# Performance work log

Hardware: AMD Instinct MI355X
Metric: run time of the kernel (lower is better)

## Reference

```python
import jax, jax.numpy as jnp
import numpy as np

B, C, H = 32, 1, 384
K = 378  # cropped size per ProbaV cPSNR spec
NSHIFT = 7  # u, v each in [0, 7)


def _crops(target):
    # 49 shifted 378x378 crops of the HR target -> [49, B, C, K, K]
    return jnp.stack([target[:, :, u:u + K, v:v + K]
                      for u in range(NSHIFT) for v in range(NSHIFT)])


def setup_inputs() -> dict:
    key = jax.random.key(0)
    k1, k2, k3 = jax.random.split(key, 3)
    # scale to [0, 255) so the HR > 5 validity mask is nontrivial
    pred = jax.random.uniform(k1, (B, C, H, H), dtype=jnp.float32) * 255.0
    target = jax.random.uniform(k2, (B, C, H, H), dtype=jnp.float32) * 255.0
    blended_target = jax.random.uniform(k3, (B, C, H, H), dtype=jnp.float32) * 255.0
    return {"pred": pred, "target": target, "blended_target": blended_target}


def reference(pred, target, blended_target):
    # SR: center crop of the super-resolved prediction
    SR = pred[:, :, 3:3 + K, 3:3 + K]                      # [B, C, K, K]
    HR = _crops(target)                                     # [49, B, C, K, K]
    mask = (HR > 5.0).astype(SR.dtype)                      # validity mask per shift
    denom = jnp.sum(mask, axis=(1, 2, 3, 4))                # [49]
    co = 1.0 / denom
    # brightness bias b per shift (masked mean of HR - SR)
    b = co * jnp.sum((HR - SR) * mask, axis=(1, 2, 3, 4))   # [49]
    diff = HR - SR - b[:, None, None, None, None]
    # NOTE: torch code sums the squared error over ALL pixels (unmasked),
    # scaled by 1/num_valid -- replicated faithfully here.
    cmses = co * jnp.sum(diff * diff, axis=(1, 2, 3, 4))    # [49]
    idx = jnp.argmin(cmses)                                  # first min, like strict '<' loop
    cMSE = cmses[idx]
    cPSNR = -10.0 * jnp.log10(cMSE)
    HR_best = HR[idx]                                        # [B, C, K, K]
    # ListedLoss('l1', reduction='mean') -> mean absolute error
    MAE = jnp.mean(jnp.abs(SR - HR_best))
    return (cPSNR, MAE)
```

## Files before the change

### kernel.cpp

```cpp
#include <hip/hip_runtime.h>
#include <math.h>

#define HH 384
#define H2 (HH*HH)
#define NIMG 32
#define KK 378
#define NSH 49
#define NTOTD 4572288.0

#define SEGW 14
#define NSEG 27
#define NSLOT 9
#define GR 2
#define TR 18
#define NTILE 21
#define NBLK1 (NIMG*NTILE)
#define NACT (NSEG*NSLOT)
#define LDS_STRIDE 386

typedef float v2f __attribute__((ext_vector_type(2)));

#define OFF_PART   0
#define OFF_ROWOUT (OFF_PART + 100*NBLK1)
#define OFF_HEAD   (OFF_ROWOUT + 12288*52)
#define OFF_TAIL   (OFF_HEAD + 32*7*6*4)
#define OFF_COLSUM (OFF_TAIL + 32*7*6*4)
#define OFF_MISC   (OFF_COLSUM + 224*4*2)

__device__ __forceinline__ float wred(float x) {
    x += __int_as_float(__builtin_amdgcn_update_dpp(0, __float_as_int(x), 0x111, 0xf, 0xf, true));
    x += __int_as_float(__builtin_amdgcn_update_dpp(0, __float_as_int(x), 0x112, 0xf, 0xf, true));
    x += __int_as_float(__builtin_amdgcn_update_dpp(0, __float_as_int(x), 0x114, 0xf, 0xf, true));
    x += __int_as_float(__builtin_amdgcn_update_dpp(0, __float_as_int(x), 0x118, 0xf, 0xf, true));
    x += __int_as_float(__builtin_amdgcn_update_dpp(0, __float_as_int(x), 0x142, 0xa, 0xf, true));
    x += __int_as_float(__builtin_amdgcn_update_dpp(0, __float_as_int(x), 0x143, 0xc, 0xf, true));
    return x;
}

__global__ __launch_bounds__(256) void k_corr(
    const float* __restrict__ pred, const float* __restrict__ targ,
    float* __restrict__ part)
{
    __shared__ v2f lds_t[(TR + 6) * LDS_STRIDE];
    __shared__ float red[100];

    const int bid = blockIdx.x;
    const int img = bid / NTILE;
    const int tile = bid - img * NTILE;
    const int r0 = tile * TR;
    const int tid = threadIdx.x;
    const int lane = tid & 63;

    if (tid < 100) red[tid] = 0.0f;

    const float* timg = targ + (size_t)img * H2;
    for (int k = 0; k < 9; ++k) {
        int i = tid + k * 256;
        int r = i / 96, c4 = (i - r * 96) * 4;
        const float4 t4 = *reinterpret_cast<const float4*>(timg + (r0 + r) * HH + c4);
        int base = r * LDS_STRIDE + c4;
        lds_t[base + 0] = (v2f){t4.x, t4.x > 5.0f ? 1.0f : 0.0f};
        lds_t[base + 1] = (v2f){t4.y, t4.y > 5.0f ? 1.0f : 0.0f};
        lds_t[base + 2] = (v2f){t4.z, t4.z > 5.0f ? 1.0f : 0.0f};
        lds_t[base + 3] = (v2f){t4.w, t4.w > 5.0f ? 1.0f : 0.0f};
    }

    const bool valid = tid < NACT;
    int seg  = valid ? tid % NSEG : NSEG - 1;
    int slot = valid ? tid / NSEG : NSLOT - 1;
    const int c0 = seg * SEGW;
    const int slot2 = slot * GR;

    float p_[GR][SEGW];
    float sp = 0.0f, sp2 = 0.0f;
    const float* pimg = pred + (size_t)img * H2;
#pragma unroll
    for (int dr = 0; dr < GR; ++dr) {
        const float* prow = pimg + (size_t)(3 + r0 + slot2 + dr) * HH + 3 + c0;
#pragma unroll
        for (int c = 0; c < SEGW; ++c) {
            float pv = prow[c];
            p_[dr][c] = pv;
            sp += pv;
            sp2 = fmaf(pv, pv, sp2);
        }
    }

    v2f acc[NSH];
#pragma unroll
    for (int i = 0; i < NSH; ++i) acc[i] = (v2f){0.0f, 0.0f};

    __syncthreads();

#pragma unroll
    for (int g = 0; g < GR + 6; ++g) {
        v2f win[SEGW + 6];
        const int wbase = (slot2 + g) * LDS_STRIDE + c0;
#pragma unroll
        for (int c = 0; c < SEGW + 6; ++c) win[c] = lds_t[wbase + c];
#pragma unroll
        for (int dr = 0; dr < GR; ++dr) {
            const int u = g - dr;
            if (u < 0 || u > 6) continue;
#pragma unroll
            for (int c = 0; c < SEGW; ++c) {
                const float pv = p_[dr][c];
                const v2f pvv = (v2f){pv, pv};
#pragma unroll
                for (int v = 0; v < 7; ++v)
                    acc[u * 7 + v] += win[v + c] * pvv;
            }
        }
        __builtin_amdgcn_sched_barrier(0);
    }

    const float vf = valid ? 1.0f : 0.0f;
    sp *= vf; sp2 *= vf;
#pragma unroll
    for (int i = 0; i < NSH; ++i) {
        float rx = wred(acc[i].x * vf);
        float ry = wred(acc[i].y * vf);
        if (lane == 63) { atomicAdd(&red[2 * i], rx); atomicAdd(&red[2 * i + 1], ry); }
    }
    {
        float rs = wred(sp), rs2 = wred(sp2);
        if (lane == 63) { atomicAdd(&red[98], rs); atomicAdd(&red[99], rs2); }
    }
    __syncthreads();
    if (tid < 100) part[(size_t)tid * NBLK1 + bid] = red[tid];
}

__global__ __launch_bounds__(256) void k_rows(
    const float* __restrict__ targ, float* __restrict__ rowout)
{
    const int tid = threadIdx.x;
    const int w = tid >> 6, lane = tid & 63;
    const int row = blockIdx.x * 4 + w;
    const int img = row / HH, y = row - img * HH;
    const float* tr = targ + (size_t)img * H2 + (size_t)y * HH;
    float* ro = rowout + (size_t)row * 52;

    float s0 = 0, s1 = 0, s2 = 0, s3 = 0;
#pragma unroll
    for (int j = 0; j < 6; ++j) {
        int x = lane + 64 * j;
        float t = tr[x];
        float m = t > 5.0f ? 1.0f : 0.0f;
        float t2 = t * t, tm = t * m;
        s0 += t; s1 += t2; s2 += tm; s3 += m;
        if (j == 0 && lane < 6) {
            ro[4 + x * 4 + 0] = t; ro[4 + x * 4 + 1] = t2;
            ro[4 + x * 4 + 2] = tm; ro[4 + x * 4 + 3] = m;
        }
        if (j == 5 && lane >= 58) {
            int k = x - 378;
            ro[28 + k * 4 + 0] = t; ro[28 + k * 4 + 1] = t2;
            ro[28 + k * 4 + 2] = tm; ro[28 + k * 4 + 3] = m;
        }
    }
    s0 = wred(s0); s1 = wred(s1); s2 = wred(s2); s3 = wred(s3);
    if (lane == 63) { ro[0] = s0; ro[1] = s1; ro[2] = s2; ro[3] = s3; }
}

__global__ __launch_bounds__(256) void k_cols(
    const float* __restrict__ rowout, double* __restrict__ colsum,
    float* __restrict__ headw, float* __restrict__ tailw)
{
    __shared__ double sd[256][4];
    const int img = blockIdx.x / 7, v = blockIdx.x - img * 7;
    const int tid = threadIdx.x;
    double a[4] = {0, 0, 0, 0};

    for (int y = tid; y < HH; y += 256) {
        const float* rp = rowout + ((size_t)img * HH + y) * 52;
        float rw[4];
#pragma unroll
        for (int q = 0; q < 4; ++q) rw[q] = rp[q];
        for (int j = 0; j < v; ++j)
#pragma unroll
            for (int q = 0; q < 4; ++q) rw[q] -= rp[4 + j * 4 + q];
        for (int k = v; k < 6; ++k)
#pragma unroll
            for (int q = 0; q < 4; ++q) rw[q] -= rp[28 + k * 4 + q];
#pragma unroll
        for (int q = 0; q < 4; ++q) a[q] += (double)rw[q];
        if (y < 6) {
#pragma unroll
            for (int q = 0; q < 4; ++q)
                headw[(((size_t)img * 7 + v) * 6 + y) * 4 + q] = rw[q];
        }
        if (y >= KK) {
#pragma unroll
            for (int q = 0; q < 4; ++q)
                tailw[(((size_t)img * 7 + v) * 6 + (y - KK)) * 4 + q] = rw[q];
        }
    }
#pragma unroll
    for (int q = 0; q < 4; ++q) sd[tid][q] = a[q];
    __syncthreads();
    if (tid < 4) {
        double t = 0;
        for (int i = 0; i < 256; ++i) t += sd[i][tid];
        colsum[((size_t)img * 7 + v) * 4 + tid] = t;
    }
}

__global__ __launch_bounds__(256) void k_comb(
    const float* __restrict__ part, const double* __restrict__ colsum,
    const float* __restrict__ headw, const float* __restrict__ tailw,
    float* __restrict__ out, int* __restrict__ misc)
{
    __shared__ double sd[200];
    __shared__ double corrD[100];
    __shared__ double Wd[NSH][4];
    const int tid = threadIdx.x;

    if (tid < 200) {
        int i = tid >> 1, h = tid & 1;
        const float* pp = part + (size_t)i * NBLK1 + h * 336;
        double s = 0;
        for (int b = 0; b < 336; ++b) s += (double)pp[b];
        sd[tid] = s;
    }
    __syncthreads();
    if (tid < 100) corrD[tid] = sd[2 * tid] + sd[2 * tid + 1];

    if (tid < 196) {
        int s = tid >> 2, q = tid & 3;
        int u = s / 7, v = s - u * 7;
        double a = 0;
        for (int img = 0; img < NIMG; ++img) {
            a += colsum[((size_t)img * 7 + v) * 4 + q];
            const float* hw = headw + (((size_t)img * 7 + v) * 6) * 4;
            const float* tw = tailw + (((size_t)img * 7 + v) * 6) * 4;
            for (int y = 0; y < u; ++y) a -= (double)hw[y * 4 + q];
            for (int k = u; k < 6; ++k) a -= (double)tw[k * 4 + q];
        }
        Wd[s][q] = a;
    }
    __syncthreads();

    if (tid == 0) {
        const double Sp = corrD[98], Sp2 = corrD[99];
        double best = 1e300; int bi = 0;
        for (int s = 0; s < NSH; ++s) {
            double tp = corrD[2 * s], mp = corrD[2 * s + 1];
            double Wt = Wd[s][0], Wt2 = Wd[s][1], Wtm = Wd[s][2], cnt = Wd[s][3];
            double b = (Wtm - mp) / cnt;
            double s1 = Wt - Sp;
            double s2t = Wt2 - 2.0 * tp + Sp2;
            double cmse = (s2t - 2.0 * b * s1 + NTOTD * b * b) / cnt;
            if (cmse < best) { best = cmse; bi = s; }
        }
        out[0] = (float)(-10.0 * log10(best));
        out[1] = 0.0f;
        misc[0] = bi;
    }
}

__global__ __launch_bounds__(256) void k_mae(
    const float* __restrict__ pred, const float* __restrict__ targ,
    const int* __restrict__ misc, float* __restrict__ out)
{
    __shared__ float ps[4];
    const int idx = misc[0];
    const int u = idx / 7, v = idx - u * 7;
    const int tid = threadIdx.x;
    const int lane = tid & 63, w = tid >> 6;
    const int total = NIMG * KK * KK;
    float s = 0.0f;
    for (int i = blockIdx.x * 256 + tid; i < total; i += gridDim.x * 256) {
        int img = i / (KK * KK);
        int rem = i - img * (KK * KK);
        int r = rem / KK, c = rem - r * KK;
        float t = targ[(size_t)img * H2 + (size_t)(r + u) * HH + (c + v)];
        float p = pred[(size_t)img * H2 + (size_t)(r + 3) * HH + (c + 3)];
        s += fabsf(t - p);
    }
    s = wred(s);
    if (lane == 63) ps[w] = s;
    __syncthreads();
    if (tid == 0)
        atomicAdd(&out[1], (ps[0] + ps[1] + ps[2] + ps[3]) * (float)(1.0 / NTOTD));
}

extern "C" void kernel_launch(void* const* d_in, const int* in_sizes, int n_in,
                              void* d_out, int out_size, void* d_ws, size_t ws_size,
                              hipStream_t stream) {
    const float* pred = (const float*)d_in[0];
    const float* targ = (const float*)d_in[1];
    float* w = (float*)d_ws;
    float* part    = w + OFF_PART;
    float* rowout  = w + OFF_ROWOUT;
    float* headw   = w + OFF_HEAD;
    float* tailw   = w + OFF_TAIL;
    double* colsum = (double*)(w + OFF_COLSUM);
    int*   misc    = (int*)(w + OFF_MISC);
    float* out = (float*)d_out;

    k_corr<<<NBLK1, 256, 0, stream>>>(pred, targ, part);
    k_rows<<<12288 / 4, 256, 0, stream>>>(targ, rowout);
    k_cols<<<NIMG * 7, 256, 0, stream>>>(rowout, colsum, headw, tailw);
    k_comb<<<1, 256, 0, stream>>>(part, colsum, headw, tailw, out, misc);
    k_mae<<<1024, 256, 0, stream>>>(pred, targ, misc, out);
}
```

Before: 222.0 us.

## Parallelize final reductions across blocks and move shift-window sums into column kernel

The single-block combine kernel, which serially summed 672 partials per correlation term and looped over images and head/tail rows, is split up. A new 100-block reduction kernel now sums the correlation partials. The column kernel now uses 384 threads, one per row, with vectorized float4 loads and a tree reduction in LDS. It also computes the per-shift window sums directly, and a small final kernel picks the argmin. This targets the serial tail latency of the one-block kernel, at the cost of an extra kernel launch and more double-precision LDS traffic.

```diff
diff --git a/kernel.cpp b/kernel.cpp
--- a/kernel.cpp
+++ b/kernel.cpp
@@ -22,10 +22,9 @@
 
 #define OFF_PART   0
 #define OFF_ROWOUT (OFF_PART + 100*NBLK1)
-#define OFF_HEAD   (OFF_ROWOUT + 12288*52)
-#define OFF_TAIL   (OFF_HEAD + 32*7*6*4)
-#define OFF_COLSUM (OFF_TAIL + 32*7*6*4)
-#define OFF_MISC   (OFF_COLSUM + 224*4*2)
+#define OFF_WPART  (OFF_ROWOUT + 12288*52)
+#define OFF_CORRD  (OFF_WPART + 12544)
+#define OFF_MISC   (OFF_CORRD + 200)
 
 __device__ __forceinline__ float wred(float x) {
     x += __int_as_float(__builtin_amdgcn_update_dpp(0, __float_as_int(x), 0x111, 0xf, 0xf, true));
@@ -162,96 +161,103 @@
     if (lane == 63) { ro[0] = s0; ro[1] = s1; ro[2] = s2; ro[3] = s3; }
 }
 
-__global__ __launch_bounds__(256) void k_cols(
-    const float* __restrict__ rowout, double* __restrict__ colsum,
-    float* __restrict__ headw, float* __restrict__ tailw)
-{
-    __shared__ double sd[256][4];
+__global__ __launch_bounds__(384) void k_cols(
+    const float* __restrict__ rowout, double* __restrict__ wpart)
+{
+    __shared__ double sd[384][4];
+    __shared__ float hb[6][4], tb[6][4];
     const int img = blockIdx.x / 7, v = blockIdx.x - img * 7;
-    const int tid = threadIdx.x;
-    double a[4] = {0, 0, 0, 0};
-
-    for (int y = tid; y < HH; y += 256) {
-        const float* rp = rowout + ((size_t)img * HH + y) * 52;
-        float rw[4];
-#pragma unroll
-        for (int q = 0; q < 4; ++q) rw[q] = rp[q];
-        for (int j = 0; j < v; ++j)
-#pragma unroll
-            for (int q = 0; q < 4; ++q) rw[q] -= rp[4 + j * 4 + q];
-        for (int k = v; k < 6; ++k)
-#pragma unroll
-            for (int q = 0; q < 4; ++q) rw[q] -= rp[28 + k * 4 + q];
-#pragma unroll
-        for (int q = 0; q < 4; ++q) a[q] += (double)rw[q];
-        if (y < 6) {
-#pragma unroll
-            for (int q = 0; q < 4; ++q)
-                headw[(((size_t)img * 7 + v) * 6 + y) * 4 + q] = rw[q];
-        }
-        if (y >= KK) {
-#pragma unroll
-            for (int q = 0; q < 4; ++q)
-                tailw[(((size_t)img * 7 + v) * 6 + (y - KK)) * 4 + q] = rw[q];
-        }
-    }
-#pragma unroll
-    for (int q = 0; q < 4; ++q) sd[tid][q] = a[q];
-    __syncthreads();
-    if (tid < 4) {
-        double t = 0;
-        for (int i = 0; i < 256; ++i) t += sd[i][tid];
-        colsum[((size_t)img * 7 + v) * 4 + tid] = t;
-    }
-}
-
-__global__ __launch_bounds__(256) void k_comb(
-    const float* __restrict__ part, const double* __restrict__ colsum,
-    const float* __restrict__ headw, const float* __restrict__ tailw,
+    const int y = threadIdx.x;
+
+    const float* rp = rowout + ((size_t)img * HH + y) * 52;
+    float4 r4[13];
+#pragma unroll
+    for (int i = 0; i < 13; ++i) r4[i] = reinterpret_cast<const float4*>(rp)[i];
+    const float* rf = reinterpret_cast<const float*>(r4);
+
+    float rw[4];
+#pragma unroll
+    for (int q = 0; q < 4; ++q) rw[q] = rf[q];
+    for (int j = 0; j < v; ++j)
+#pragma unroll
+        for (int q = 0; q < 4; ++q) rw[q] -= rf[4 + j * 4 + q];
+    for (int k = v; k < 6; ++k)
+#pragma unroll
+        for (int q = 0; q < 4; ++q) rw[q] -= rf[28 + k * 4 + q];
+
+#pragma unroll
+    for (int q = 0; q < 4; ++q) sd[y][q] = (double)rw[q];
+    if (y < 6)
+#pragma unroll
+        for (int q = 0; q < 4; ++q) hb[y][q] = rw[q];
+    if (y >= KK)
+#pragma unroll
+        for (int q = 0; q < 4; ++q) tb[y - KK][q] = rw[q];
+    __syncthreads();
+
+    for (int s = 192; s >= 3; s >>= 1) {
+        if (y < s)
+#pragma unroll
+            for (int q = 0; q < 4; ++q) sd[y][q] += sd[y + s][q];
+        __syncthreads();
+    }
+
+    if (y < 28) {
+        int u = y >> 2, q = y & 3;
+        double a = sd[0][q] + sd[1][q] + sd[2][q];
+        for (int j = 0; j < u; ++j) a -= (double)hb[j][q];
+        for (int k = u; k < 6; ++k) a -= (double)tb[k][q];
+        wpart[((size_t)(u * 7 + v) * 4 + q) * 32 + img] = a;
+    }
+}
+
+__global__ __launch_bounds__(256) void k_red(
+    const float* __restrict__ part, double* __restrict__ corrD)
+{
+    __shared__ double sd[256];
+    const int q = blockIdx.x;
+    const int t = threadIdx.x;
+    const float* pp = part + (size_t)q * NBLK1;
+    double a = (double)pp[t] + (double)pp[t + 256];
+    if (t < NBLK1 - 512) a += (double)pp[t + 512];
+    sd[t] = a;
+    __syncthreads();
+    for (int s = 128; s > 0; s >>= 1) {
+        if (t < s) sd[t] += sd[t + s];
+        __syncthreads();
+    }
+    if (t == 0) corrD[q] = sd[0];
+}
+
+__global__ __launch_bounds__(256) void k_fin(
+    const double* __restrict__ corrD, const double* __restrict__ wpart,
     float* __restrict__ out, int* __restrict__ misc)
 {
-    __shared__ double sd[200];
-    __shared__ double corrD[100];
     __shared__ double Wd[NSH][4];
-    const int tid = threadIdx.x;
-
-    if (tid < 200) {
-        int i = tid >> 1, h = tid & 1;
-        const float* pp = part + (size_t)i * NBLK1 + h * 336;
-        double s = 0;
-        for (int b = 0; b < 336; ++b) s += (double)pp[b];
-        sd[tid] = s;
-    }
-    __syncthreads();
-    if (tid < 100) corrD[tid] = sd[2 * tid] + sd[2 * tid + 1];
-
-    if (tid < 196) {
-        int s = tid >> 2, q = tid & 3;
-        int u = s / 7, v = s - u * 7;
-        double a = 0;
-        for (int img = 0; img < NIMG; ++img) {
-            a += colsum[((size_t)img * 7 + v) * 4 + q];
-            const float* hw = headw + (((size_t)img * 7 + v) * 6) * 4;
-            const float* tw = tailw + (((size_t)img * 7 + v) * 6) * 4;
-            for (int y = 0; y < u; ++y) a -= (double)hw[y * 4 + q];
-            for (int k = u; k < 6; ++k) a -= (double)tw[k * 4 + q];
-        }
-        Wd[s][q] = a;
-    }
-    __syncthreads();
-
-    if (tid == 0) {
-        const double Sp = corrD[98], Sp2 = corrD[99];
-        double best = 1e300; int bi = 0;
-        for (int s = 0; s < NSH; ++s) {
-            double tp = corrD[2 * s], mp = corrD[2 * s + 1];
-            double Wt = Wd[s][0], Wt2 = Wd[s][1], Wtm = Wd[s][2], cnt = Wd[s][3];
-            double b = (Wtm - mp) / cnt;
-            double s1 = Wt - Sp;
-            double s2t = Wt2 - 2.0 * tp + Sp2;
-            double cmse = (s2t - 2.0 * b * s1 + NTOTD * b * b) / cnt;
-            if (cmse < best) { best = cmse; bi = s; }
-        }
+    __shared__ double cm[NSH];
+    const int t = threadIdx.x;
+
+    if (t < 196) {
+        const double* wp = wpart + (size_t)t * 32;
+        double a0 = 0, a1 = 0;
+#pragma unroll
+        for (int i = 0; i < 32; i += 2) { a0 += wp[i]; a1 += wp[i + 1]; }
+        Wd[t >> 2][t & 3] = a0 + a1;
+    }
+    __syncthreads();
+    if (t < NSH) {
+        double tp = corrD[2 * t], mp = corrD[2 * t + 1];
+        double Sp = corrD[98], Sp2 = corrD[99];
+        double b = (Wd[t][2] - mp) / Wd[t][3];
+        double s1 = Wd[t][0] - Sp;
+        double s2t = Wd[t][1] - 2.0 * tp + Sp2;
+        cm[t] = (s2t - 2.0 * b * s1 + NTOTD * b * b) / Wd[t][3];
+    }
+    __syncthreads();
+    if (t == 0) {
+        double best = cm[0]; int bi = 0;
+        for (int s = 1; s < NSH; ++s)
+            if (cm[s] < best) { best = cm[s]; bi = s; }
         out[0] = (float)(-10.0 * log10(best));
         out[1] = 0.0f;
         misc[0] = bi;
@@ -290,17 +296,17 @@
     const float* pred = (const float*)d_in[0];
     const float* targ = (const float*)d_in[1];
     float* w = (float*)d_ws;
-    float* part    = w + OFF_PART;
-    float* rowout  = w + OFF_ROWOUT;
-    float* headw   = w + OFF_HEAD;
-    float* tailw   = w + OFF_TAIL;
-    double* colsum = (double*)(w + OFF_COLSUM);
-    int*   misc    = (int*)(w + OFF_MISC);
+    float*  part   = w + OFF_PART;
+    float*  rowout = w + OFF_ROWOUT;
+    double* wpart  = (double*)(w + OFF_WPART);
+    double* corrD  = (double*)(w + OFF_CORRD);
+    int*    misc   = (int*)(w + OFF_MISC);
     float* out = (float*)d_out;
 
     k_corr<<<NBLK1, 256, 0, stream>>>(pred, targ, part);
     k_rows<<<12288 / 4, 256, 0, stream>>>(targ, rowout);
-    k_cols<<<NIMG * 7, 256, 0, stream>>>(rowout, colsum, headw, tailw);
-    k_comb<<<1, 256, 0, stream>>>(part, colsum, headw, tailw, out, misc);
+    k_cols<<<NIMG * 7, 384, 0, stream>>>(rowout, wpart);
+    k_red<<<100, 256, 0, stream>>>(part, corrD);
+    k_fin<<<1, 256, 0, stream>>>(corrD, wpart, out, misc);
     k_mae<<<1024, 256, 0, stream>>>(pred, targ, misc, out);
 }
```

Result: faster. 180.5 us (-18.7%).
